# Kernel optimization log

Measured on AMD Instinct MI355X. Metric: run time of the kernel, lower is better.

Reference implementation:

```python
import jax, jax.numpy as jnp
import numpy as np

K = 12  # nsample_k; graph per point has K nodes (self + K-1 abs-diff neighbors)


def setup_inputs() -> dict:
    key = jax.random.key(0)
    k1, k2, k3 = jax.random.split(key, 3)
    p = jax.random.normal(k1, (2, 8192, 3), dtype=jnp.float32)
    W = jax.random.normal(k2, (1, 3), dtype=jnp.float32) * 0.5  # GCNConv lin weight [out=1, in=3]
    b = jax.random.normal(k3, (1,), dtype=jnp.float32) * 0.1    # GCNConv bias
    return {"p": p, "W": W, "b": b}


def _knn_idx(pts, k):
    # k nearest neighbors over the whole flattened cloud, self included then dropped
    pts = jax.lax.stop_gradient(pts)  # indices are non-differentiable
    sq = jnp.sum(pts * pts, axis=-1)                      # [n]
    d2 = sq[:, None] + sq[None, :] - 2.0 * (pts @ pts.T)  # [n, n] squared distances
    _, idx = jax.lax.top_k(-d2, k)                        # ascending distance
    return idx[:, 1:]                                     # drop self -> [n, k-1]


def reference(p, W, b):
    # p: [B, N, 3] -> flatten to [n, 3]
    pts = p.reshape(-1, 3)
    nidx = _knn_idx(pts, K)            # [n, K-1]
    nbr = pts[nidx]                    # [n, K-1, 3]
    # node features of each star graph: node 0 = point, nodes 1..K-1 = |p - neighbor|
    p_ij = jnp.concatenate([pts[:, None, :], jnp.abs(pts[:, None, :] - nbr)], axis=1)  # [n, K, 3]
    # GCNConv(3,1) on identical star graphs (edges 0->j, plus self loops), closed form:
    #   deg0 = 1, deg_j = 2  =>  out0 = x0 W^T + b ; out_j = x0 W^T / sqrt(2) + x_j W^T / 2 + b
    xw = jnp.einsum('nkc,oc->nko', p_ij, W)  # [n, K, 1]
    inv_s2 = 1.0 / jnp.sqrt(jnp.float32(2.0))
    out0 = xw[:, :1] + b                                  # [n, 1, 1]
    outj = inv_s2 * xw[:, :1] + 0.5 * xw[:, 1:] + b       # [n, K-1, 1]
    emb = jnp.concatenate([out0, outj], axis=1)           # [n, K, 1]
    # POOL: squeeze -> [n, K]; AdaptiveAvgPool1d(1) -> [n, 1]; module returns avg only
    return jnp.mean(emb[..., 0], axis=1, keepdims=True)   # [n, 1]
```

## Files before the change

### kernel.cpp

```cpp
#include <hip/hip_runtime.h>
#include <math.h>


#define NBINS  2048
#define PARTS  16
#define CMIN_  (-6.0f)
#define INVBW_ ((float)NBINS / 12.0f)
#define BLOCK  256
#define WPB    4
#define SEED   768
#define KK     12
#define CD     4
#define BIG    3.0e38f

__device__ __forceinline__ int bin_of(float x) {
  int b = (int)((x - CMIN_) * INVBW_);
  b = b < 0 ? 0 : b;
  b = b > NBINS - 1 ? NBINS - 1 : b;
  return b;
}

__device__ __forceinline__ float wave_min(float v) {
#pragma unroll
  for (int o = 1; o < 64; o <<= 1) v = fminf(v, __shfl_xor(v, o));
  return v;
}

__device__ __forceinline__ void ins4(float (&qd)[CD], float (&qw)[CD],
                                     float d, float w) {
#pragma unroll
  for (int k = CD - 1; k >= 1; --k) {
    const bool up  = (qd[k - 1] > d);
    const bool mid = (qd[k] > d);
    const float nd = up ? qd[k - 1] : (mid ? d : qd[k]);
    const float nw = up ? qw[k - 1] : (mid ? w : qw[k]);
    qd[k] = nd; qw[k] = nw;
  }
  if (qd[0] > d) { qw[0] = w; qd[0] = d; }
}

__global__ __launch_bounds__(1024)
void sort_kernel(const float* __restrict__ p, int* __restrict__ c_all,
                 float4* __restrict__ s_all, int n) {
  __shared__ int h_all[NBINS];
  __shared__ int h_pre[NBINS];
  __shared__ int wsum[16];
  const int tid  = threadIdx.x;
  const int dim  = blockIdx.x / PARTS;
  const int part = blockIdx.x % PARTS;
  const int chunk   = (n + PARTS - 1) / PARTS;
  const int myStart = part * chunk;
  const int myEnd   = min(myStart + chunk, n);

  h_all[tid] = 0; h_all[tid + 1024] = 0;
  h_pre[tid] = 0; h_pre[tid + 1024] = 0;
  __syncthreads();

  for (int i = tid; i < n; i += 1024) {
    const int b = bin_of(p[3 * i + dim]);
    atomicAdd(&h_all[b], 1);
    if (i < myStart) atomicAdd(&h_pre[b], 1);
  }
  __syncthreads();

  const int a = h_all[2 * tid], b = h_all[2 * tid + 1];
  const int v = a + b;
  const int lane = tid & 63, wid = tid >> 6;
  int incl = v;
#pragma unroll
  for (int o = 1; o < 64; o <<= 1) {
    const int t = __shfl_up(incl, o);
    if (lane >= o) incl += t;
  }
  if (lane == 63) wsum[wid] = incl;
  __syncthreads();
  int woff = 0;
  for (int wI = 0; wI < wid; ++wI) woff += wsum[wI];
  const int excl = woff + incl - v;

  if (part == 0) {
    int* __restrict__ cursor = c_all + (size_t)dim * NBINS;
    cursor[2 * tid]     = excl + a;
    cursor[2 * tid + 1] = excl + a + b;
  }

  const int c0 = excl + h_pre[2 * tid];
  const int c1 = excl + a + h_pre[2 * tid + 1];
  __syncthreads();
  h_pre[2 * tid]     = c0;
  h_pre[2 * tid + 1] = c1;
  __syncthreads();

  float4* __restrict__ sorted = s_all + (size_t)dim * n;
  for (int i = myStart + tid; i < myEnd; i += 1024) {
    const float x = p[3 * i], y = p[3 * i + 1], z = p[3 * i + 2];
    const float c = (dim == 0) ? x : (dim == 1) ? y : z;
    const int pos = atomicAdd(&h_pre[bin_of(c)], 1);
    sorted[pos] = make_float4(x, y, z, __int_as_float(i));
  }
}

__global__ __launch_bounds__(BLOCK, 1)
void query_kernel(const float4* __restrict__ sx, const float4* __restrict__ sy,
                  const float4* __restrict__ sz, const int* __restrict__ cx,
                  const int* __restrict__ cy, const int* __restrict__ cz,
                  const float* __restrict__ W, const float* __restrict__ bias,
                  float* __restrict__ out, int n) {
  const int lane = threadIdx.x & 63;
  const int wv   = threadIdx.x >> 6;
  const int t    = wv * (n >> 2) + blockIdx.x;
  const float W0 = W[0], W1 = W[1], W2 = W[2];
  const float bb = bias[0];

  const float4 me = sx[t];
  const float xi = me.x, yi = me.y, zi = me.z;
  const int orig = __float_as_int(me.w);

  const float ax = fabsf(xi), ay = fabsf(yi), az = fabsf(zi);
  const float4* sv; const int* cur; float cq;
  if (ay >= ax && ay >= az)      { sv = sy; cur = cy; cq = yi; }
  else if (az >= ax && az >= ay) { sv = sz; cur = cz; cq = zi; }
  else                           { sv = sx; cur = cx; cq = xi; }

  const int bq = bin_of(cq);
  const int bs = (bq > 0) ? cur[bq - 1] : 0;
  const int be = cur[bq];
  int lo = ((bs + be) >> 1) - SEED / 2;
  lo = lo < 0 ? 0 : lo;
  lo = lo > n - SEED ? n - SEED : lo;
  const float4* base = sv + lo + lane;

  float4 cs[SEED / 64];
#pragma unroll
  for (int s = 0; s < SEED / 64; ++s) cs[s] = base[s * 64];
  float m0 = BIG, m1 = BIG, m2 = BIG, m3 = BIG;
#pragma unroll
  for (int s = 0; s < SEED / 64; s += 4) {
    {
      const float dx = xi - cs[s].x, dy = yi - cs[s].y, dz = zi - cs[s].z;
      m0 = fminf(m0, fmaf(dx, dx, fmaf(dy, dy, dz * dz)));
    }
    {
      const float dx = xi - cs[s + 1].x, dy = yi - cs[s + 1].y, dz = zi - cs[s + 1].z;
      m1 = fminf(m1, fmaf(dx, dx, fmaf(dy, dy, dz * dz)));
    }
    {
      const float dx = xi - cs[s + 2].x, dy = yi - cs[s + 2].y, dz = zi - cs[s + 2].z;
      m2 = fminf(m2, fmaf(dx, dx, fmaf(dy, dy, dz * dz)));
    }
    {
      const float dx = xi - cs[s + 3].x, dy = yi - cs[s + 3].y, dz = zi - cs[s + 3].z;
      m3 = fminf(m3, fmaf(dx, dx, fmaf(dy, dy, dz * dz)));
    }
  }
  const float m = fminf(fminf(m0, m1), fminf(m2, m3));

  float u;
  {
    float v = m;
#pragma unroll
    for (int r = 0; r < KK; ++r) {
      const float mm = wave_min(v);
      u = mm;
      v = (v == mm) ? BIG : v;
    }
  }

  const float s = sqrtf(u);
  const int bl = bin_of(cq - s);
  const int bh = bin_of(cq + s);
  const int lo2 = (bl > 0) ? cur[bl - 1] : 0;
  const int hi2 = cur[bh];
  const int len   = hi2 - lo2;
  const int full  = len >> 6;
  const int steps = (len + 63) >> 6;

  float qd[CD], qw[CD];
  int ccnt = 0;
#pragma unroll
  for (int k = 0; k < CD; ++k) { qd[k] = BIG; qw[k] = 0.f; }

#define PROC1(c)                                                              \
  {                                                                           \
    const float dx = xi - (c).x, dy = yi - (c).y, dz = zi - (c).z;            \
    const float d2 = fmaf(dx, dx, fmaf(dy, dy, dz * dz));                     \
    if (d2 <= u) {                                                            \
      const float w = fmaf(W0, fabsf(dx), fmaf(W1, fabsf(dy), W2 * fabsf(dz)));\
      ++ccnt; ins4(qd, qw, d2, w);                                            \
    }                                                                         \
  }

  const float4* cbase = sv + lo2 + lane;
  int st = 0;
  for (; st + 4 <= full; st += 4) {
    const float4 c0 = cbase[(st + 0) * 64];
    const float4 c1 = cbase[(st + 1) * 64];
    const float4 c2 = cbase[(st + 2) * 64];
    const float4 c3 = cbase[(st + 3) * 64];
    PROC1(c0) PROC1(c1) PROC1(c2) PROC1(c3)
  }
  for (; st < full; ++st) {
    const float4 c = cbase[st * 64];
    PROC1(c)
  }
  if (st < steps) {
    const int pos = lo2 + st * 64 + lane;
    if (pos < hi2) {
      const float4 c = sv[pos];
      PROC1(c)
    }
  }
#undef PROC1

  float acc = 0.f;
  const bool ovf = __ballot(ccnt > CD) != 0ULL;
  if (!ovf) {
#pragma unroll
    for (int r = 0; r < KK; ++r) {
      const float mm = wave_min(qd[0]);
      const unsigned long long bal = __ballot(qd[0] == mm);
      if (qd[0] == mm && lane == (int)(__ffsll(bal) - 1)) {
        acc += qw[0];
#pragma unroll
        for (int k = 0; k < CD - 1; ++k) { qd[k] = qd[k + 1]; qw[k] = qw[k + 1]; }
        qd[CD - 1] = BIG;
      }
    }
  } else {
    float dd[KK];
#pragma unroll
    for (int k = 0; k < KK; ++k) dd[k] = BIG;
    for (int s0 = 0; s0 < steps; ++s0) {
      const int pos = lo2 + s0 * 64 + lane;
      const float4 c = sv[(pos < hi2) ? pos : hi2 - 1];
      const float dx = xi - c.x, dy = yi - c.y, dz = zi - c.z;
      const float d2 = (pos < hi2) ? fmaf(dx, dx, fmaf(dy, dy, dz * dz)) : BIG;
#pragma unroll
      for (int k = KK - 1; k >= 1; --k)
        dd[k] = __builtin_amdgcn_fmed3f(d2, dd[k - 1], dd[k]);
      dd[0] = fminf(dd[0], d2);
    }
    float tau = 0.f;
#pragma unroll
    for (int r = 0; r < KK; ++r) {
      const float mm = wave_min(dd[0]);
      if (dd[0] == mm) {
#pragma unroll
        for (int k = 0; k < KK - 1; ++k) dd[k] = dd[k + 1];
        dd[KK - 1] = BIG;
      }
      tau = mm;
    }
    for (int s0 = 0; s0 < steps; ++s0) {
      const int pos = lo2 + s0 * 64 + lane;
      if (pos < hi2) {
        const float4 c = sv[pos];
        const float dx = xi - c.x, dy = yi - c.y, dz = zi - c.z;
        const float d2 = fmaf(dx, dx, fmaf(dy, dy, dz * dz));
        const float w  = fmaf(W0, fabsf(dx), fmaf(W1, fabsf(dy), W2 * fabsf(dz)));
        acc += (d2 <= tau) ? w : 0.f;
      }
    }
  }

#pragma unroll
  for (int o = 1; o < 64; o <<= 1) acc += __shfl_xor(acc, o);
  if (lane == 0) {
    const float xw0 = W0 * xi + W1 * yi + W2 * zi;
    out[orig] = bb + (xw0 * 8.778174593052022f + 0.5f * acc) * (1.0f / 12.0f);
  }
}

extern "C" void kernel_launch(void* const* d_in, const int* in_sizes, int n_in,
                              void* d_out, int out_size, void* d_ws, size_t ws_size,
                              hipStream_t stream) {
  const float* p  = (const float*)d_in[0];
  const float* W  = (const float*)d_in[1];
  const float* bb = (const float*)d_in[2];
  float* out = (float*)d_out;

  const int n = in_sizes[0] / 3;

  int*    c_all = (int*)d_ws;
  float4* s_all = (float4*)((char*)d_ws + 3 * NBINS * 4);
  int*    cx = c_all;
  int*    cy = cx + NBINS;
  int*    cz = cy + NBINS;
  float4* sx = s_all;
  float4* sy = sx + n;
  float4* sz = sy + n;

  sort_kernel<<<3 * PARTS, 1024, 0, stream>>>(p, c_all, s_all, n);
  query_kernel<<<n / WPB, BLOCK, 0, stream>>>(sx, sy, sz, cx, cy, cz, W, bb, out, n);
}
```

Baseline: 120.0 us.

## Bisect kNN radius via ballot count and double-buffer candidate loads

Replaces the 12-round wave-min extraction of the seed radius with a max reduction followed by 10 bisection steps that count lanes under a threshold with ballot/popcount. Rewrites the candidate scan as a software-pipelined, double-buffered loop that prefetches the next four chunks while processing the current four, using clamped indices and masking instead of a separate tail path. Adds a scheduling barrier after the seed loads. The bisected radius is an upper bound, slightly looser than the exact 12th minimum, so more candidates may pass the filter and trigger the overflow path. The loop also always loads and processes at least four chunks, even when the range is short.

```diff
diff --git a/kernel.cpp b/kernel.cpp
--- a/kernel.cpp
+++ b/kernel.cpp
@@ -133,6 +133,7 @@
   float4 cs[SEED / 64];
 #pragma unroll
   for (int s = 0; s < SEED / 64; ++s) cs[s] = base[s * 64];
+  __builtin_amdgcn_sched_barrier(0);
   float m0 = BIG, m1 = BIG, m2 = BIG, m3 = BIG;
 #pragma unroll
   for (int s = 0; s < SEED / 64; s += 4) {
@@ -157,13 +158,17 @@
 
   float u;
   {
-    float v = m;
-#pragma unroll
-    for (int r = 0; r < KK; ++r) {
-      const float mm = wave_min(v);
-      u = mm;
-      v = (v == mm) ? BIG : v;
-    }
+    float hiv = m;
+#pragma unroll
+    for (int o = 1; o < 64; o <<= 1) hiv = fmaxf(hiv, __shfl_xor(hiv, o));
+    float lov = 0.f;
+#pragma unroll
+    for (int it = 0; it < 10; ++it) {
+      const float mid = 0.5f * (lov + hiv);
+      const int cnt = __popcll(__ballot(m <= mid));
+      if (cnt >= KK) hiv = mid; else lov = mid;
+    }
+    u = hiv;
   }
 
   const float s = sqrtf(u);
@@ -172,45 +177,43 @@
   const int lo2 = (bl > 0) ? cur[bl - 1] : 0;
   const int hi2 = cur[bh];
   const int len   = hi2 - lo2;
-  const int full  = len >> 6;
-  const int steps = (len + 63) >> 6;
+  const int nch   = (len + 63) >> 6;
+  const int steps = nch;
 
   float qd[CD], qw[CD];
   int ccnt = 0;
 #pragma unroll
   for (int k = 0; k < CD; ++k) { qd[k] = BIG; qw[k] = 0.f; }
 
-#define PROC1(c)                                                              \
+#define LD1(cix) (sv[lo2 + min((cix) * 64 + lane, len - 1)])
+#define PROCC(cc, cix)                                                        \
   {                                                                           \
-    const float dx = xi - (c).x, dy = yi - (c).y, dz = zi - (c).z;            \
-    const float d2 = fmaf(dx, dx, fmaf(dy, dy, dz * dz));                     \
+    const float dx = xi - (cc).x, dy = yi - (cc).y, dz = zi - (cc).z;         \
+    float d2 = fmaf(dx, dx, fmaf(dy, dy, dz * dz));                           \
+    d2 = ((cix) * 64 + lane < len) ? d2 : BIG;                                \
     if (d2 <= u) {                                                            \
       const float w = fmaf(W0, fabsf(dx), fmaf(W1, fabsf(dy), W2 * fabsf(dz)));\
       ++ccnt; ins4(qd, qw, d2, w);                                            \
     }                                                                         \
   }
 
-  const float4* cbase = sv + lo2 + lane;
-  int st = 0;
-  for (; st + 4 <= full; st += 4) {
-    const float4 c0 = cbase[(st + 0) * 64];
-    const float4 c1 = cbase[(st + 1) * 64];
-    const float4 c2 = cbase[(st + 2) * 64];
-    const float4 c3 = cbase[(st + 3) * 64];
-    PROC1(c0) PROC1(c1) PROC1(c2) PROC1(c3)
-  }
-  for (; st < full; ++st) {
-    const float4 c = cbase[st * 64];
-    PROC1(c)
-  }
-  if (st < steps) {
-    const int pos = lo2 + st * 64 + lane;
-    if (pos < hi2) {
-      const float4 c = sv[pos];
-      PROC1(c)
-    }
-  }
-#undef PROC1
+  {
+    float4 A0 = LD1(0), A1 = LD1(1), A2 = LD1(2), A3 = LD1(3);
+    float4 B0, B1, B2, B3;
+    int c = 0;
+    for (;;) {
+      B0 = LD1(c + 4); B1 = LD1(c + 5); B2 = LD1(c + 6); B3 = LD1(c + 7);
+      PROCC(A0, c) PROCC(A1, c + 1) PROCC(A2, c + 2) PROCC(A3, c + 3)
+      c += 4;
+      if (c >= nch) break;
+      A0 = LD1(c + 4); A1 = LD1(c + 5); A2 = LD1(c + 6); A3 = LD1(c + 7);
+      PROCC(B0, c) PROCC(B1, c + 1) PROCC(B2, c + 2) PROCC(B3, c + 3)
+      c += 4;
+      if (c >= nch) break;
+    }
+  }
+#undef LD1
+#undef PROCC
 
   float acc = 0.f;
   const bool ovf = __ballot(ccnt > CD) != 0ULL;
```

New measurement: 115.2 us. 1.04x faster.
